# Kernel optimization log

Measured on AMD Instinct MI355X. Metric: run time of the kernel, lower is better.

## Reference

```python
import jax, jax.numpy as jnp
import numpy as np

K = 3        # kernel_size
PAD = 1      # padding ('same' for stride 1)
RANK = 53    # CP rank from compression=10: round(27*32*64/(10*(9+32+64)))


def _kaiming_uniform(key, shape, fan_in):
    # matches nn.init.kaiming_uniform_(a=sqrt(5)): bound = 1/sqrt(fan_in)
    bound = 1.0 / np.sqrt(fan_in)
    return jax.random.uniform(key, shape, jnp.float32, -bound, bound)


def setup_inputs() -> dict:
    key = jax.random.key(0)
    ks = jax.random.split(key, 7)
    B, Cin, Cout, H, W, D = 1, 32, 64, 56, 56, 56
    x = jax.random.normal(ks[0], (B, Cin, H, W, D), jnp.float32)
    # CP factor matrices (fan_in = second dim for torch's 2D kaiming)
    U_kh = _kaiming_uniform(ks[1], (K, RANK), RANK)
    U_kw = _kaiming_uniform(ks[2], (K, RANK), RANK)
    U_kd = _kaiming_uniform(ks[3], (K, RANK), RANK)
    U_cin = _kaiming_uniform(ks[4], (Cin, RANK), RANK)
    U_cout = _kaiming_uniform(ks[5], (RANK, Cout), Cout)
    bias = jax.random.normal(ks[6], (Cout,), jnp.float32)
    return {"x": x, "U_kh": U_kh, "U_kw": U_kw, "U_kd": U_kd,
            "U_cin": U_cin, "U_cout": U_cout, "bias": bias}


def reference(x, U_kh, U_kw, U_kd, U_cin, U_cout, bias):
    B, C, H, W, D = x.shape
    xp = jnp.pad(x, ((0, 0), (0, 0), (PAD, PAD), (PAD, PAD), (PAD, PAD)))
    # im2col patches: patches[i,j,l,b,c,x,y,z] = xp[b,c,x+i,y+j,z+l]
    # (same values/ordering as torch unfold(2).unfold(3).unfold(4), stride=1)
    patches = jnp.stack([
        xp[:, :, i:i + H, j:j + W, l:l + D]
        for i in range(K) for j in range(K) for l in range(K)
    ]).reshape(K, K, K, B, C, H, W, D)
    # CP tensor-network contraction (legs: k_h,k_w,k_d,c_in share rank r -> c_out)
    out = jnp.einsum('ijlbcxyz,ir,jr,lr,cr,ro->boxyz',
                     patches, U_kh, U_kw, U_kd, U_cin, U_cout,
                     optimize=True)
    return out + bias[None, :, None, None, None]
```

## Files before the change

### kernel.cpp

```cpp
#include <hip/hip_runtime.h>


#define NP 175616
#define NP2 87808
#define HSTR 3136
#define H2 1568
#define W2 28
#define CIN 32
#define RK 53
#define RC0 27
#define COUT 64
#define SCR 53

__global__ __launch_bounds__(256) void k0_t(const float* __restrict__ Ucin,
                                            float* __restrict__ Ut)
{
    int t = blockIdx.x * 256 + threadIdx.x;
    if (t < RK * CIN) {
        int r = t >> 5, c = t & 31;
        Ut[t] = Ucin[c * RK + r];
    }
}

__global__ __launch_bounds__(256) void k1d(
    const float* __restrict__ x, const float* __restrict__ Ut,
    const float* __restrict__ Ukd, float* __restrict__ T1d)
{
    const int lane = threadIdx.x & 63;
    const int row  = blockIdx.x * 4 + (threadIdx.x >> 6);
    const int p    = row * 56 + lane;
    const bool act = (lane < 56);
    const int pc   = act ? p : (p - 8);

    float xv[CIN];
#pragma unroll
    for (int c = 0; c < CIN; ++c) xv[c] = x[c * NP + pc];
#pragma unroll
    for (int c = 0; c < CIN; ++c) asm volatile("" : "+v"(xv[c]));

    const int r0 = blockIdx.y ? RC0 : 0;
    const int r1 = blockIdx.y ? RK  : RC0;

#pragma unroll 2
    for (int r = r0; r < r1; ++r) {
        const float* U = Ut + r * CIN;
        float acc = 0.f;
#pragma unroll
        for (int c = 0; c < CIN; ++c) acc += xv[c] * U[c];
        float lm = __shfl_up(acc, 1, 64);
        float rp = __shfl_down(acc, 1, 64);
        if (lane == 0)  lm = 0.f;
        if (lane == 55) rp = 0.f;
        float res = lm * Ukd[r] + acc * Ukd[RK + r] + rp * Ukd[2 * RK + r];
        if (act) T1d[(size_t)r * NP + p] = res;
    }
}

__global__ __launch_bounds__(512, 4) void k3c(
    const float2* __restrict__ Ta, const float* __restrict__ Ucout,
    const float* __restrict__ bias, const float* __restrict__ Ukh,
    const float* __restrict__ Ukw, float2* __restrict__ Out)
{
    __shared__ float2 tld[RC0][64];

    const int lane = threadIdx.x & 63;
    const int wv   = threadIdx.x >> 6;

    const int nwg = gridDim.x;
    const int qx = nwg >> 3, rx = nwg & 7;
    const int xcd = blockIdx.x & 7, loc = blockIdx.x >> 3;
    const int swz = ((xcd < rx) ? xcd * (qx + 1) : rx * (qx + 1) + (xcd - rx) * qx) + loc;

    const int q  = swz * 64 + lane;
    const int h  = q / H2;
    const int rm = q - h * H2;
    const int w  = rm / W2;
    const int om = (h > 0)  ? -H2 : 0;
    const int op = (h < 55) ?  H2 : 0;
    const int oa = (w > 0)  ? -W2 : 0;
    const int oc = (w < 55) ?  W2 : 0;
    const float mh0 = (h > 0)  ? 1.f : 0.f;
    const float mh2 = (h < 55) ? 1.f : 0.f;
    const float mw0 = (w > 0)  ? 1.f : 0.f;
    const float mw2 = (w < 55) ? 1.f : 0.f;

    const float2* Sq = Ta + q;
    const int og = __builtin_amdgcn_readfirstlane(wv << 3);

    float2 a[8];

#pragma unroll 1
    for (int r = wv; r < RC0; r += 8) {
        const float2* S = Sq + (size_t)r * NP2;
        const float kw0 = mw0 * Ukw[r];
        const float kw1 = Ukw[RK + r];
        const float kw2 = mw2 * Ukw[2 * RK + r];
        const float kh0 = mh0 * Ukh[r];
        const float kh1 = Ukh[RK + r];
        const float kh2 = mh2 * Ukh[2 * RK + r];
        float2 v00 = S[om + oa], v01 = S[om], v02 = S[om + oc];
        float2 v10 = S[oa],      v11 = S[0],  v12 = S[oc];
        float2 v20 = S[op + oa], v21 = S[op], v22 = S[op + oc];
        float2 t;
        t.x = (v00.x * kw0 + v01.x * kw1 + v02.x * kw2) * kh0
            + (v10.x * kw0 + v11.x * kw1 + v12.x * kw2) * kh1
            + (v20.x * kw0 + v21.x * kw1 + v22.x * kw2) * kh2;
        t.y = (v00.y * kw0 + v01.y * kw1 + v02.y * kw2) * kh0
            + (v10.y * kw0 + v11.y * kw1 + v12.y * kw2) * kh1
            + (v20.y * kw0 + v21.y * kw1 + v22.y * kw2) * kh2;
        tld[r][lane] = t;
    }
    __syncthreads();

#pragma unroll
    for (int o = 0; o < 8; ++o) {
        float b = bias[og + o];
        a[o].x = b; a[o].y = b;
    }
#pragma unroll 4
    for (int r = 0; r < RC0; ++r) {
        float2 t = tld[r][lane];
        const float* Ur = Ucout + r * COUT + og;
#pragma unroll
        for (int o = 0; o < 8; ++o) {
            float u = Ur[o];
            a[o].x += t.x * u; a[o].y += t.y * u;
        }
    }
    __syncthreads();

#pragma unroll 1
    for (int r = RC0 + wv; r < RK; r += 8) {
        const float2* S = Sq + (size_t)r * NP2;
        const float kw0 = mw0 * Ukw[r];
        const float kw1 = Ukw[RK + r];
        const float kw2 = mw2 * Ukw[2 * RK + r];
        const float kh0 = mh0 * Ukh[r];
        const float kh1 = Ukh[RK + r];
        const float kh2 = mh2 * Ukh[2 * RK + r];
        float2 v00 = S[om + oa], v01 = S[om], v02 = S[om + oc];
        float2 v10 = S[oa],      v11 = S[0],  v12 = S[oc];
        float2 v20 = S[op + oa], v21 = S[op], v22 = S[op + oc];
        float2 t;
        t.x = (v00.x * kw0 + v01.x * kw1 + v02.x * kw2) * kh0
            + (v10.x * kw0 + v11.x * kw1 + v12.x * kw2) * kh1
            + (v20.x * kw0 + v21.x * kw1 + v22.x * kw2) * kh2;
        t.y = (v00.y * kw0 + v01.y * kw1 + v02.y * kw2) * kh0
            + (v10.y * kw0 + v11.y * kw1 + v12.y * kw2) * kh1
            + (v20.y * kw0 + v21.y * kw1 + v22.y * kw2) * kh2;
        tld[r - RC0][lane] = t;
    }
    __syncthreads();

#pragma unroll 4
    for (int r = RC0; r < RK; ++r) {
        float2 t = tld[r - RC0][lane];
        const float* Ur = Ucout + r * COUT + og;
#pragma unroll
        for (int o = 0; o < 8; ++o) {
            float u = Ur[o];
            a[o].x += t.x * u; a[o].y += t.y * u;
        }
    }

#pragma unroll
    for (int o = 0; o < 8; ++o)
        Out[(size_t)(og + o) * NP2 + q] = a[o];
}


__global__ __launch_bounds__(256) void k1_chunk(
    const float* __restrict__ x, const float* __restrict__ Ucin,
    float* T, int r0, int nr)
{
    __shared__ float sU[11 * CIN];
    const int tid = threadIdx.x;
    for (int t = tid; t < nr * CIN; t += 256) {
        int lr = t >> 5, c = t & 31;
        sU[t] = Ucin[c * RK + (r0 + lr)];
    }
    __syncthreads();
    const int p = blockIdx.x * 256 + tid;
    float xv[CIN];
#pragma unroll
    for (int c = 0; c < CIN; ++c) xv[c] = x[c * NP + p];
#pragma unroll 1
    for (int lr = 0; lr < nr; ++lr) {
        float acc = 0.f;
#pragma unroll
        for (int c = 0; c < CIN; ++c) acc += xv[c] * sU[lr * CIN + c];
        T[(size_t)(SCR + lr) * NP + p] = acc;
    }
}

__global__ __launch_bounds__(256) void k2_chunk(
    const float* __restrict__ Ukh, const float* __restrict__ Ukw,
    const float* __restrict__ Ukd, float* T, int r0)
{
    __shared__ float sIn[5800];
    __shared__ float sA[5600];
    const int lr = blockIdx.z;
    const int r  = r0 + lr;
    const int h0 = blockIdx.x * 8, w0 = blockIdx.y * 8;
    const int tid = threadIdx.x;
    const float kh0 = Ukh[r], kh1 = Ukh[RK + r], kh2 = Ukh[2 * RK + r];
    const float kw0 = Ukw[r], kw1 = Ukw[RK + r], kw2 = Ukw[2 * RK + r];
    const float kd0 = Ukd[r], kd1 = Ukd[RK + r], kd2 = Ukd[2 * RK + r];
    const float* T1r = T + (size_t)(SCR + lr) * NP;

    for (int idx = tid; idx < 5800; idx += 256) {
        int d = idx % 58; int t2 = idx / 58; int ww = t2 % 10; int hh = t2 / 10;
        int gh = h0 + hh - 1, gw = w0 + ww - 1, gd = d - 1;
        float v = 0.f;
        if ((unsigned)gh < 56u && (unsigned)gw < 56u && (unsigned)gd < 56u)
            v = T1r[gh * HSTR + gw * 56 + gd];
        sIn[idx] = v;
    }
    __syncthreads();
    for (int idx = tid; idx < 5600; idx += 256) {
        int d = idx % 56; int t2 = idx / 56; int ww = t2 % 10; int hh = t2 / 10;
        const float* b = &sIn[(hh * 10 + ww) * 58 + d];
        sA[idx] = b[0] * kd0 + b[1] * kd1 + b[2] * kd2;
    }
    __syncthreads();
    const float k00 = kh0 * kw0, k01 = kh0 * kw1, k02 = kh0 * kw2;
    const float k10 = kh1 * kw0, k11 = kh1 * kw1, k12 = kh1 * kw2;
    const float k20 = kh2 * kw0, k21 = kh2 * kw1, k22 = kh2 * kw2;
    for (int idx = tid; idx < 3584; idx += 256) {
        int d = idx % 56; int t2 = idx / 56; int ww = t2 % 8; int hh = t2 / 8;
        const float* a = &sA[(hh * 10 + ww) * 56 + d];
        float acc = a[0]    * k00 + a[56]   * k01 + a[112]  * k02
                  + a[560]  * k10 + a[616]  * k11 + a[672]  * k12
                  + a[1120] * k20 + a[1176] * k21 + a[1232] * k22;
        T[(size_t)r * NP + (h0 + hh) * HSTR + (w0 + ww) * 56 + d] = acc;
    }
}

__global__ __launch_bounds__(256) void k3_out(
    float* T, const float* __restrict__ Ucout, const float* __restrict__ bias)
{
    __shared__ float sUo[RK * COUT];
    __shared__ float sB[COUT];
    const int tid = threadIdx.x;
    for (int t = tid; t < RK * COUT; t += 256) sUo[t] = Ucout[t];
    if (tid < COUT) sB[tid] = bias[tid];
    __syncthreads();
    const int p = blockIdx.x * 256 + tid;
    float acc[COUT];
#pragma unroll
    for (int o = 0; o < COUT; ++o) acc[o] = sB[o];
#pragma unroll 1
    for (int r = 0; r < RK; ++r) {
        float t = T[(size_t)r * NP + p];
        const float* Ur = &sUo[r * COUT];
#pragma unroll
        for (int o = 0; o < COUT; ++o) acc[o] += t * Ur[o];
    }
#pragma unroll
    for (int o = 0; o < COUT; ++o) T[(size_t)o * NP + p] = acc[o];
}


extern "C" void kernel_launch(void* const* d_in, const int* in_sizes, int n_in,
                              void* d_out, int out_size, void* d_ws, size_t ws_size,
                              hipStream_t stream)
{
    const float* x     = (const float*)d_in[0];
    const float* Ukh   = (const float*)d_in[1];
    const float* Ukw   = (const float*)d_in[2];
    const float* Ukd   = (const float*)d_in[3];
    const float* Ucin  = (const float*)d_in[4];
    const float* Ucout = (const float*)d_in[5];
    const float* bias  = (const float*)d_in[6];

    const size_t t1_bytes = (size_t)RK * NP * sizeof(float);

    if (ws_size >= t1_bytes + 8192) {
        float* T1 = (float*)d_ws;
        float* Ut = (float*)((char*)d_ws + t1_bytes);
        k0_t<<<7, 256, 0, stream>>>(Ucin, Ut);
        k1d<<<dim3(HSTR / 4, 2), 256, 0, stream>>>(x, Ut, Ukd, T1);
        k3c<<<NP2 / 64, 512, 0, stream>>>((const float2*)T1, Ucout, bias, Ukh,
                                          Ukw, (float2*)d_out);
    } else {
        float* T = (float*)d_out;
        for (int r0 = 0; r0 < RK; r0 += 11) {
            int nr = (RK - r0 < 11) ? (RK - r0) : 11;
            k1_chunk<<<NP / 256, 256, 0, stream>>>(x, Ucin, T, r0, nr);
            k2_chunk<<<dim3(7, 7, nr), 256, 0, stream>>>(Ukh, Ukw, Ukd, T, r0);
        }
        k3_out<<<NP / 256, 256, 0, stream>>>(T, Ucout, bias);
    }
}
```

Baseline: 140.6 us.

## Split k1d rank loop into 9 chunks of 6 with batched shuffles and ILP

The rank dimension of the first-stage kernel is split into 9 grid slices of 6 ranks instead of 2 slices of about 27. Each thread computes up to 6 rank dot-products with four independent accumulators, then issues all lane shuffles together before the depthwise combine and store. Launch bounds request higher occupancy. The intent is more parallelism and latency hiding in this write-bound stage, at the cost of re-reading x nine times instead of twice.

```diff
diff --git a/kernel.cpp b/kernel.cpp
--- a/kernel.cpp
+++ b/kernel.cpp
@@ -22,7 +22,7 @@
     }
 }
 
-__global__ __launch_bounds__(256) void k1d(
+__global__ __launch_bounds__(256, 8) void k1d(
     const float* __restrict__ x, const float* __restrict__ Ut,
     const float* __restrict__ Ukd, float* __restrict__ T1d)
 {
@@ -38,21 +38,44 @@
 #pragma unroll
     for (int c = 0; c < CIN; ++c) asm volatile("" : "+v"(xv[c]));
 
-    const int r0 = blockIdx.y ? RC0 : 0;
-    const int r1 = blockIdx.y ? RK  : RC0;
-
-#pragma unroll 2
-    for (int r = r0; r < r1; ++r) {
-        const float* U = Ut + r * CIN;
-        float acc = 0.f;
-#pragma unroll
-        for (int c = 0; c < CIN; ++c) acc += xv[c] * U[c];
-        float lm = __shfl_up(acc, 1, 64);
-        float rp = __shfl_down(acc, 1, 64);
-        if (lane == 0)  lm = 0.f;
-        if (lane == 55) rp = 0.f;
-        float res = lm * Ukd[r] + acc * Ukd[RK + r] + rp * Ukd[2 * RK + r];
-        if (act) T1d[(size_t)r * NP + p] = res;
+    const int r0 = blockIdx.y * 6;
+    const int nr = (r0 + 6 <= RK) ? 6 : (RK - r0);
+
+    float acc[6];
+#pragma unroll
+    for (int rr = 0; rr < 6; ++rr) {
+        if (rr < nr) {
+            const float* U = Ut + (r0 + rr) * CIN;
+            float a0 = 0.f, a1 = 0.f, a2 = 0.f, a3 = 0.f;
+#pragma unroll
+            for (int c = 0; c < CIN; c += 4) {
+                a0 += xv[c]     * U[c];
+                a1 += xv[c + 1] * U[c + 1];
+                a2 += xv[c + 2] * U[c + 2];
+                a3 += xv[c + 3] * U[c + 3];
+            }
+            acc[rr] = (a0 + a1) + (a2 + a3);
+        }
+    }
+
+    float lm[6], rp[6];
+#pragma unroll
+    for (int rr = 0; rr < 6; ++rr) {
+        if (rr < nr) {
+            lm[rr] = __shfl_up(acc[rr], 1, 64);
+            rp[rr] = __shfl_down(acc[rr], 1, 64);
+        }
+    }
+
+#pragma unroll
+    for (int rr = 0; rr < 6; ++rr) {
+        if (rr < nr) {
+            const int r = r0 + rr;
+            float l  = (lane == 0)  ? 0.f : lm[rr];
+            float rv = (lane == 55) ? 0.f : rp[rr];
+            float res = l * Ukd[r] + acc[rr] * Ukd[RK + r] + rv * Ukd[2 * RK + r];
+            if (act) T1d[(size_t)r * NP + p] = res;
+        }
     }
 }
 
@@ -279,7 +302,7 @@
         float* T1 = (float*)d_ws;
         float* Ut = (float*)((char*)d_ws + t1_bytes);
         k0_t<<<7, 256, 0, stream>>>(Ucin, Ut);
-        k1d<<<dim3(HSTR / 4, 2), 256, 0, stream>>>(x, Ut, Ukd, T1);
+        k1d<<<dim3(HSTR / 4, 9), 256, 0, stream>>>(x, Ut, Ukd, T1);
         k3c<<<NP2 / 64, 512, 0, stream>>>((const float2*)T1, Ucout, bias, Ukh,
                                           Ukw, (float2*)d_out);
     } else {
```

Result: slower. 143.5 us (+2.1%).
